# Kernel optimization log

Hardware: AMD Instinct MI355X
Metric: run time of the kernel (lower is better)

The kernel has to match this reference:

```python
import jax, jax.numpy as jnp
import numpy as np
from jax import lax

B, S, E = 8, 2048, 1024
NH, K = 4, 4
DH = E // NH  # 256


def setup_inputs() -> dict:
    key = jax.random.key(0)
    ks = jax.random.split(key, 8)
    sc = 0.02  # small_init-style scale
    return {
        "x": jax.random.normal(ks[0], (B, S, E), jnp.float32),
        "conv_w": jax.random.normal(ks[1], (K, 1, E), jnp.float32) * sc,  # depthwise (W,1,E)
        "conv_b": jnp.zeros((E,), jnp.float32),
        "fgate_w": jax.random.normal(ks[2], (NH, DH, DH), jnp.float32) * sc,
        "igate_w": jax.random.normal(ks[3], (NH, DH, DH), jnp.float32) * sc,
        "zgate_w": jax.random.normal(ks[4], (NH, DH, DH), jnp.float32) * sc,
        "ogate_w": jax.random.normal(ks[5], (NH, DH, DH), jnp.float32) * sc,
        "rkernel": jax.random.normal(ks[6], (NH, DH, 4 * DH), jnp.float32) * sc,
        "rbias": jnp.zeros((NH, 4, DH), jnp.float32),
        "gn_weight": jnp.ones((E,), jnp.float32),
    }


def _headwise(x, w):
    # LinearHeadwiseExpand, bias=False: einsum('...hd,hod->...ho')
    Bx, Sx, _ = x.shape
    return jnp.einsum('bshd,hod->bsho', x.reshape(Bx, Sx, NH, DH), w)


def reference(x, conv_w, conv_b, fgate_w, igate_w, zgate_w, ogate_w, rkernel, rbias, gn_weight):
    # --- causal depthwise conv1d + SiLU ---
    xp = jnp.pad(x, ((0, 0), (K - 1, 0), (0, 0)))  # left pad -> causal
    xc = lax.conv_general_dilated(
        xp, conv_w, window_strides=(1,), padding='VALID',
        dimension_numbers=('NWC', 'WIO', 'NWC'), feature_group_count=E) + conv_b
    x_conv = xc * jax.nn.sigmoid(xc)  # SiLU

    # --- headwise gate pre-activations (matches torch cat order [i,f,z,o]) ---
    gi = _headwise(x_conv, fgate_w)
    gf = _headwise(x_conv, igate_w)
    gz = _headwise(x, zgate_w)
    go = _headwise(x, ogate_w)
    gx = jnp.stack([gi, gf, gz, go], axis=3)      # (B,S,NH,4,DH)
    gx_t = jnp.moveaxis(gx, 1, 0)                 # (S,B,NH,4,DH)

    # --- stabilized exponential-gated sLSTM recurrence (xLSTM vanilla cell) ---
    z0 = jnp.zeros((B, NH, DH), x.dtype)

    def step(carry, xt):
        y, c, n, m = carry  # each (B,NH,DH)
        ry = jnp.einsum('bhd,hdk->bhk', y, rkernel).reshape(B, NH, 4, DH)
        raw = xt + ry + rbias
        ir, fr, zr, orr = raw[:, :, 0], raw[:, :, 1], raw[:, :, 2], raw[:, :, 3]
        logfplusm = m + jax.nn.log_sigmoid(fr)
        mnew = jnp.maximum(ir, logfplusm)
        ig = jnp.exp(ir - mnew)
        fg = jnp.exp(logfplusm - mnew)
        cnew = fg * c + ig * jnp.tanh(zr)
        nnew = fg * n + ig
        ynew = jax.nn.sigmoid(orr) * cnew / nnew
        return (ynew, cnew, nnew, mnew), ynew

    _, ys = lax.scan(step, (z0, z0, z0, z0), gx_t)  # ys: (S,B,NH,DH)
    y = jnp.moveaxis(ys, 0, 1)                       # (B,S,NH,DH)

    # --- MultiHeadLayerNorm: group_norm with num_groups=NH, weight only (no bias) ---
    mu = jnp.mean(y, axis=-1, keepdims=True)
    var = jnp.var(y, axis=-1, keepdims=True)
    yn = (y - mu) * lax.rsqrt(var + 1e-5)
    out = (yn * gn_weight.reshape(NH, DH)).reshape(B, S, E)
    return out
```

## Files before the change

kernel.cpp:

```cpp
#include <hip/hip_runtime.h>
#include <hip/hip_fp16.h>

#define BB 8
#define SS 2048
#define EE 1024
#define NHH 4
#define DHH 256

typedef _Float16 f16x2 __attribute__((ext_vector_type(2)));

__device__ __forceinline__ __half2 u2h2(unsigned int u) {
  union { unsigned int u; __half2 h; } c; c.u = u; return c.h;
}
__device__ __forceinline__ unsigned int h2u(__half2 h) {
  union { unsigned int u; __half2 h; } c; c.h = h; return c.u;
}
__device__ __forceinline__ f16x2 u2f(unsigned int u) {
  union { unsigned int u; f16x2 f; } c; c.u = u; return c.f;
}
__device__ __forceinline__ unsigned int pack2(float a, float b) {
  f16x2 f; f.x = (_Float16)a; f.y = (_Float16)b;
  union { f16x2 f; unsigned int u; } c; c.f = f; return c.u;
}
__device__ __forceinline__ float fdot2u(unsigned int w, unsigned int y, float acc) {
#if __has_builtin(__builtin_amdgcn_fdot2)
  return __builtin_amdgcn_fdot2(u2f(w), u2f(y), acc, false);
#else
  __half2 a = u2h2(w), b = u2h2(y);
  return acc + __low2float(a) * __low2float(b) + __high2float(a) * __high2float(b);
#endif
}

__global__ __launch_bounds__(256) void gates_gemm(
    const float* __restrict__ x, const float* __restrict__ conv_w,
    const float* __restrict__ conv_b,
    const float* __restrict__ fgw, const float* __restrict__ igw,
    const float* __restrict__ zgw, const float* __restrict__ ogw,
    __half* __restrict__ gx)
{
  __shared__ float Xs[67][33];
  __shared__ float As[64][33];
  __shared__ float Bs[32][68];

  const int tid = threadIdx.x;
  const int mt = blockIdx.x;
  const int nt = blockIdx.y;
  const int p  = blockIdx.z;
  const int h  = p >> 1, pair = p & 1;
  const int b  = mt >> 5;
  const int s0 = (mt & 31) << 6;
  const int n0 = nt << 6;

  const float* W0 = pair ? zgw : fgw;
  const float* W1 = pair ? ogw : igw;

  const int tx = tid & 15, ty = tid >> 4;
  float acc[4][4] = {};

  for (int d0 = 0; d0 < DHH; d0 += 32) {
    for (int i = tid; i < 67 * 32; i += 256) {
      int r = i >> 5, c = i & 31;
      int s = s0 - 3 + r;
      float v = 0.f;
      if (s >= 0) v = x[((size_t)b * SS + s) * EE + h * DHH + d0 + c];
      Xs[r][c] = v;
    }
    for (int i = tid; i < 32 * 64; i += 256) {
      int j = i >> 5, c = i & 31;
      int o = n0 + j;
      const float* Wp = (o < 256) ? W0 : W1;
      int oo = o & 255;
      Bs[c][j] = Wp[((size_t)h * DHH + oo) * DHH + d0 + c];
    }
    __syncthreads();
    if (pair == 0) {
      for (int i = tid; i < 64 * 32; i += 256) {
        int r = i >> 5, c = i & 31;
        int e = h * DHH + d0 + c;
        float xc = conv_b[e];
        xc = fmaf(Xs[r + 0][c], conv_w[0 * EE + e], xc);
        xc = fmaf(Xs[r + 1][c], conv_w[1 * EE + e], xc);
        xc = fmaf(Xs[r + 2][c], conv_w[2 * EE + e], xc);
        xc = fmaf(Xs[r + 3][c], conv_w[3 * EE + e], xc);
        float sg = 1.f / (1.f + __expf(-xc));
        As[r][c] = xc * sg;
      }
    } else {
      for (int i = tid; i < 64 * 32; i += 256) {
        int r = i >> 5, c = i & 31;
        As[r][c] = Xs[r + 3][c];
      }
    }
    __syncthreads();
#pragma unroll
    for (int kk = 0; kk < 32; ++kk) {
      float a[4];
#pragma unroll
      for (int i = 0; i < 4; ++i) a[i] = As[ty * 4 + i][kk];
      float4 bv = *(const float4*)&Bs[kk][tx * 4];
      float bb[4] = {bv.x, bv.y, bv.z, bv.w};
#pragma unroll
      for (int i = 0; i < 4; ++i)
#pragma unroll
        for (int j = 0; j < 4; ++j)
          acc[i][j] = fmaf(a[i], bb[j], acc[i][j]);
    }
    __syncthreads();
  }

#pragma unroll
  for (int i = 0; i < 4; ++i) {
    int s = s0 + ty * 4 + i;
    size_t base = (((size_t)s * BB + b) * NHH + h) * 1024 + (size_t)pair * 512 + n0 + tx * 4;
    uint2 st;
    st.x = h2u(__floats2half2_rn(acc[i][0], acc[i][1]));
    st.y = h2u(__floats2half2_rn(acc[i][2], acc[i][3]));
    *(uint2*)(gx + base) = st;
  }
}

__global__
__attribute__((amdgpu_flat_work_group_size(512, 512), amdgpu_waves_per_eu(1)))
void slstm_scan(
    const float* __restrict__ rk,
    const float* __restrict__ rb,
    const __half* __restrict__ gx,
    float* __restrict__ out)
{
  extern __shared__ unsigned char smem[];
  uint4* wl4   = (uint4*)smem;
  __half* ypub = (__half*)(smem + 131072);

  const int t = threadIdx.x;
  const int b = blockIdx.x >> 2, h = blockIdx.x & 3;
  const int d = t >> 1, par = t & 1;
  const int kbase = par << 7;
  const float* Rh = rk + (size_t)h * DHH * 1024;

  unsigned int wv[3][64];
#pragma unroll
  for (int g = 0; g < 3; ++g) {
    const int col = g * 256 + d;
#pragma unroll
    for (int pp = 0; pp < 64; ++pp) {
      int k = kbase + 2 * pp;
      wv[g][pp] = pack2(Rh[(size_t)k * 1024 + col], Rh[(size_t)(k + 1) * 1024 + col]);
    }
  }
  {
    const int col = 3 * 256 + d;
    for (int q = 0; q < 16; ++q) {
      uint4 u;
      int k = kbase + 8 * q;
      u.x = pack2(Rh[(size_t)(k + 0) * 1024 + col], Rh[(size_t)(k + 1) * 1024 + col]);
      u.y = pack2(Rh[(size_t)(k + 2) * 1024 + col], Rh[(size_t)(k + 3) * 1024 + col]);
      u.z = pack2(Rh[(size_t)(k + 4) * 1024 + col], Rh[(size_t)(k + 5) * 1024 + col]);
      u.w = pack2(Rh[(size_t)(k + 6) * 1024 + col], Rh[(size_t)(k + 7) * 1024 + col]);
      wl4[q * 512 + t] = u;
    }
  }

  float rbv[4];
#pragma unroll
  for (int g = 0; g < 4; ++g) rbv[g] = rb[h * 1024 + g * 256 + d];

  float c = 0.f, n = 0.f, m = 0.f;
  if (t < 256) { ypub[t] = __float2half(0.f); ypub[256 + t] = __float2half(0.f); }
  __syncthreads();

  int cur = 0;
  const __half* pg = gx + ((size_t)b * NHH + h) * 1024;
  float cx[4];
#pragma unroll
  for (int g = 0; g < 4; ++g) cx[g] = __half2float(pg[g * 256 + d]);
  const size_t out_base = ((size_t)b * SS) * EE + h * DHH + d;

  for (int st = 0; st < SS; ++st) {
    const __half* pn = pg + ((st + 1 < SS) ? (size_t)(BB * NHH * 1024) : 0);
    __half nx[4];
#pragma unroll
    for (int g = 0; g < 4; ++g) nx[g] = pn[g * 256 + d];

    const uint4* yv = (const uint4*)(ypub + cur * 256) + (par << 4);
    float aA0 = 0.f, aB0 = 0.f, aA1 = 0.f, aB1 = 0.f;
    float aA2 = 0.f, aB2 = 0.f, aA3 = 0.f, aB3 = 0.f;
#pragma unroll
    for (int j = 0; j < 16; ++j) {
      uint4 yq = yv[j];
      uint4 wq = wl4[j * 512 + t];
      aA0 = fdot2u(wv[0][4 * j + 0], yq.x, aA0);
      aA1 = fdot2u(wv[1][4 * j + 0], yq.x, aA1);
      aA2 = fdot2u(wv[2][4 * j + 0], yq.x, aA2);
      aA3 = fdot2u(wq.x,             yq.x, aA3);
      aB0 = fdot2u(wv[0][4 * j + 1], yq.y, aB0);
      aB1 = fdot2u(wv[1][4 * j + 1], yq.y, aB1);
      aB2 = fdot2u(wv[2][4 * j + 1], yq.y, aB2);
      aB3 = fdot2u(wq.y,             yq.y, aB3);
      aA0 = fdot2u(wv[0][4 * j + 2], yq.z, aA0);
      aA1 = fdot2u(wv[1][4 * j + 2], yq.z, aA1);
      aA2 = fdot2u(wv[2][4 * j + 2], yq.z, aA2);
      aA3 = fdot2u(wq.z,             yq.z, aA3);
      aB0 = fdot2u(wv[0][4 * j + 3], yq.w, aB0);
      aB1 = fdot2u(wv[1][4 * j + 3], yq.w, aB1);
      aB2 = fdot2u(wv[2][4 * j + 3], yq.w, aB2);
      aB3 = fdot2u(wq.w,             yq.w, aB3);
    }

    float part0 = aA0 + aB0, part1 = aA1 + aB1;
    float part2 = aA2 + aB2, part3 = aA3 + aB3;
    float raw0 = part0 + __shfl_xor(part0, 1) + cx[0] + rbv[0];
    float raw1 = part1 + __shfl_xor(part1, 1) + cx[1] + rbv[1];
    float raw2 = part2 + __shfl_xor(part2, 1) + cx[2] + rbv[2];
    float raw3 = part3 + __shfl_xor(part3, 1) + cx[3] + rbv[3];

    float iv = raw0, fv = raw1, zv = raw2, ov = raw3;
    float ea = __expf(-fabsf(fv));
    float ls = fminf(fv, 0.f) - __logf(1.f + ea);
    float lfm = m + ls;
    float mn = fmaxf(iv, lfm);
    float ig = __expf(iv - mn);
    float fg = __expf(lfm - mn);
    float pz = __expf(-2.f * fabsf(zv));
    float tmag = __fdividef(1.f - pz, 1.f + pz);
    float th = (zv < 0.f) ? -tmag : tmag;
    c = fg * c + ig * th;
    n = fg * n + ig;
    float og = __fdividef(1.f, 1.f + __expf(-ov));
    float y = og * __fdividef(c, n);
    m = mn;

    if (par == 0) {
      out[out_base + (size_t)st * EE] = y;
      ypub[(cur ^ 1) * 256 + d] = __float2half(y);
    }
    __syncthreads();
    cur ^= 1;
    pg = pn;
#pragma unroll
    for (int g = 0; g < 4; ++g) cx[g] = __half2float(nx[g]);
  }
}

__global__ __launch_bounds__(256) void groupnorm(
    float* __restrict__ y, const float* __restrict__ gnw)
{
  const int row = blockIdx.x;
  const int t = threadIdx.x;
  float4 v = ((const float4*)y)[(size_t)row * 256 + t];
  float s = v.x + v.y + v.z + v.w;
  float q = v.x * v.x + v.y * v.y + v.z * v.z + v.w * v.w;
#pragma unroll
  for (int mask = 1; mask < 64; mask <<= 1) {
    s += __shfl_xor(s, mask, 64);
    q += __shfl_xor(q, mask, 64);
  }
  float mu = s * (1.f / 256.f);
  float var = q * (1.f / 256.f) - mu * mu;
  float rs = rsqrtf(var + 1e-5f);
  float4 g = ((const float4*)gnw)[t];
  float4 o;
  o.x = (v.x - mu) * rs * g.x;
  o.y = (v.y - mu) * rs * g.y;
  o.z = (v.z - mu) * rs * g.z;
  o.w = (v.w - mu) * rs * g.w;
  ((float4*)y)[(size_t)row * 256 + t] = o;
}

extern "C" void kernel_launch(void* const* d_in, const int* in_sizes, int n_in,
                              void* d_out, int out_size, void* d_ws, size_t ws_size,
                              hipStream_t stream) {
  const float* x      = (const float*)d_in[0];
  const float* conv_w = (const float*)d_in[1];
  const float* conv_b = (const float*)d_in[2];
  const float* fgw    = (const float*)d_in[3];
  const float* igw    = (const float*)d_in[4];
  const float* zgw    = (const float*)d_in[5];
  const float* ogw    = (const float*)d_in[6];
  const float* rk     = (const float*)d_in[7];
  const float* rb     = (const float*)d_in[8];
  const float* gnw    = (const float*)d_in[9];
  float* out = (float*)d_out;
  __half* gx = (__half*)d_ws;

  dim3 g1(256, 8, 8);
  gates_gemm<<<g1, 256, 0, stream>>>(x, conv_w, conv_b, fgw, igw, zgw, ogw, gx);

  const int scan_lds = 131072 + 1024;
  (void)hipFuncSetAttribute(reinterpret_cast<const void*>(slstm_scan),
                            hipFuncAttributeMaxDynamicSharedMemorySize, scan_lds);
  slstm_scan<<<32, 512, scan_lds, stream>>>(rk, rb, gx, out);

  groupnorm<<<BB * SS, 256, 0, stream>>>(out, gnw);
}
```

Measured before the change: 4.292 ms.

## Use MFMA f16 matrix cores for gate GEMM with seq-major tiling

Rewrites the gate pre-activation GEMM to use the 16x16x32 f16 MFMA instruction instead of scalar FP32 FMAs. Operands are converted to half in shared memory. The M tile is re-laid out as 8 timesteps by 8 batches, so output rows map directly onto the (S,B) layout of gx. This cuts the arithmetic cost of the GEMM stage, at the price of f16 input rounding and narrower scalar half stores. The sequential scan kernel likely dominates total time, so the overall effect may be limited.

```diff
diff --git a/kernel.cpp b/kernel.cpp
--- a/kernel.cpp
+++ b/kernel.cpp
@@ -8,6 +8,8 @@
 #define DHH 256
 
 typedef _Float16 f16x2 __attribute__((ext_vector_type(2)));
+typedef _Float16 f16x8 __attribute__((ext_vector_type(8)));
+typedef float f32x4 __attribute__((ext_vector_type(4)));
 
 __device__ __forceinline__ __half2 u2h2(unsigned int u) {
   union { unsigned int u; __half2 h; } c; c.u = u; return c.h;
@@ -38,84 +40,86 @@
     const float* __restrict__ zgw, const float* __restrict__ ogw,
     __half* __restrict__ gx)
 {
-  __shared__ float Xs[67][33];
-  __shared__ float As[64][33];
-  __shared__ float Bs[32][68];
+  __shared__ float Xs[8][11][33];
+  __shared__ __half As[64][40];
+  __shared__ __half Bs[64][40];
 
   const int tid = threadIdx.x;
   const int mt = blockIdx.x;
   const int nt = blockIdx.y;
   const int p  = blockIdx.z;
   const int h  = p >> 1, pair = p & 1;
-  const int b  = mt >> 5;
-  const int s0 = (mt & 31) << 6;
+  const int s0 = mt << 3;
   const int n0 = nt << 6;
 
   const float* W0 = pair ? zgw : fgw;
   const float* W1 = pair ? ogw : igw;
 
-  const int tx = tid & 15, ty = tid >> 4;
-  float acc[4][4] = {};
+  const int w = tid >> 6, l = tid & 63;
+  const int lrow = l & 15, kq = l >> 4;
+  const int koff = kq << 3;
+
+  f32x4 acc[4] = {};
 
   for (int d0 = 0; d0 < DHH; d0 += 32) {
-    for (int i = tid; i < 67 * 32; i += 256) {
-      int r = i >> 5, c = i & 31;
-      int s = s0 - 3 + r;
-      float v = 0.f;
-      if (s >= 0) v = x[((size_t)b * SS + s) * EE + h * DHH + d0 + c];
-      Xs[r][c] = v;
-    }
-    for (int i = tid; i < 32 * 64; i += 256) {
-      int j = i >> 5, c = i & 31;
-      int o = n0 + j;
-      const float* Wp = (o < 256) ? W0 : W1;
-      int oo = o & 255;
-      Bs[c][j] = Wp[((size_t)h * DHH + oo) * DHH + d0 + c];
-    }
-    __syncthreads();
+    const int ebase = h * DHH + d0;
+
     if (pair == 0) {
+      for (int i = tid; i < 8 * 11 * 32; i += 256) {
+        int kk = i & 31, rest = i >> 5;
+        int b = rest / 11, si = rest - b * 11;
+        int sg = s0 - 3 + si;
+        float v = 0.f;
+        if (sg >= 0) v = x[((size_t)b * SS + sg) * EE + ebase + kk];
+        Xs[b][si][kk] = v;
+      }
+      __syncthreads();
       for (int i = tid; i < 64 * 32; i += 256) {
-        int r = i >> 5, c = i & 31;
-        int e = h * DHH + d0 + c;
+        int kk = i & 31, r = i >> 5;
+        int sl = r >> 3, b = r & 7;
+        int e = ebase + kk;
         float xc = conv_b[e];
-        xc = fmaf(Xs[r + 0][c], conv_w[0 * EE + e], xc);
-        xc = fmaf(Xs[r + 1][c], conv_w[1 * EE + e], xc);
-        xc = fmaf(Xs[r + 2][c], conv_w[2 * EE + e], xc);
-        xc = fmaf(Xs[r + 3][c], conv_w[3 * EE + e], xc);
+        xc = fmaf(Xs[b][sl + 0][kk], conv_w[0 * EE + e], xc);
+        xc = fmaf(Xs[b][sl + 1][kk], conv_w[1 * EE + e], xc);
+        xc = fmaf(Xs[b][sl + 2][kk], conv_w[2 * EE + e], xc);
+        xc = fmaf(Xs[b][sl + 3][kk], conv_w[3 * EE + e], xc);
         float sg = 1.f / (1.f + __expf(-xc));
-        As[r][c] = xc * sg;
+        As[r][kk] = __float2half(xc * sg);
       }
     } else {
       for (int i = tid; i < 64 * 32; i += 256) {
-        int r = i >> 5, c = i & 31;
-        As[r][c] = Xs[r + 3][c];
+        int kk = i & 31, r = i >> 5;
+        int sl = r >> 3, b = r & 7;
+        As[r][kk] = __float2half(x[((size_t)b * SS + s0 + sl) * EE + ebase + kk]);
       }
     }
+    for (int i = tid; i < 64 * 32; i += 256) {
+      int k = i & 31, col = i >> 5;
+      int o = n0 + col;
+      const float* Wp = (o < 256) ? W0 : W1;
+      int oo = o & 255;
+      Bs[col][k] = __float2half(Wp[((size_t)h * DHH + oo) * DHH + d0 + k]);
+    }
     __syncthreads();
-#pragma unroll
-    for (int kk = 0; kk < 32; ++kk) {
-      float a[4];
-#pragma unroll
-      for (int i = 0; i < 4; ++i) a[i] = As[ty * 4 + i][kk];
-      float4 bv = *(const float4*)&Bs[kk][tx * 4];
-      float bb[4] = {bv.x, bv.y, bv.z, bv.w};
-#pragma unroll
-      for (int i = 0; i < 4; ++i)
-#pragma unroll
-        for (int j = 0; j < 4; ++j)
-          acc[i][j] = fmaf(a[i], bb[j], acc[i][j]);
+
+    f16x8 bfrag = *(const f16x8*)&Bs[w * 16 + lrow][koff];
+#pragma unroll
+    for (int mtl = 0; mtl < 4; ++mtl) {
+      f16x8 afrag = *(const f16x8*)&As[mtl * 16 + lrow][koff];
+      acc[mtl] = __builtin_amdgcn_mfma_f32_16x16x32_f16(afrag, bfrag, acc[mtl], 0, 0, 0);
     }
     __syncthreads();
   }
 
 #pragma unroll
-  for (int i = 0; i < 4; ++i) {
-    int s = s0 + ty * 4 + i;
-    size_t base = (((size_t)s * BB + b) * NHH + h) * 1024 + (size_t)pair * 512 + n0 + tx * 4;
-    uint2 st;
-    st.x = h2u(__floats2half2_rn(acc[i][0], acc[i][1]));
-    st.y = h2u(__floats2half2_rn(acc[i][2], acc[i][3]));
-    *(uint2*)(gx + base) = st;
+  for (int mtl = 0; mtl < 4; ++mtl) {
+#pragma unroll
+    for (int j = 0; j < 4; ++j) {
+      int row_loc = mtl * 16 + kq * 4 + j;
+      int grow = s0 * 8 + row_loc;
+      int colg = n0 + w * 16 + lrow;
+      gx[(size_t)grow * 4096 + h * 1024 + pair * 512 + colg] = __float2half(acc[mtl][j]);
+    }
   }
 }
 
```

Measured after the change: 3.958 ms. 7.8% less time.
